# Kernel optimization log

Hardware: AMD Instinct MI355X
Metric: run time of the kernel (lower is better)

The kernel has to match this reference:

```python
import jax, jax.numpy as jnp
import numpy as np

MARGIN = 0.5   # arcface additive angular margin m
SCALE = 64.0   # arcface logit scale s
EPS = 1e-12    # torch F.normalize eps


def setup_inputs() -> dict:
    key = jax.random.key(0)
    k1, k2, k3 = jax.random.split(key, 3)
    B, D, C = 512, 512, 200000
    embeddings = jax.random.normal(k1, (B, D), dtype=jnp.float32)
    labels = jax.random.randint(k2, (B,), 0, C, dtype=jnp.int64)
    weight = 0.01 * jax.random.normal(k3, (C, D), dtype=jnp.float32)
    return {"embeddings": embeddings, "labels": labels, "weight": weight}


def _l2norm(x):
    # torch.nn.functional.normalize(x, dim=1): x / max(||x||, eps)
    n = jnp.sqrt(jnp.sum(x * x, axis=1, keepdims=True))
    return x / jnp.maximum(n, EPS)


def reference(embeddings, labels, weight):
    B = embeddings.shape[0]
    labels = labels.astype(jnp.int32)
    valid = labels >= 0                      # ignore_index=-1 semantics
    safe = jnp.where(valid, labels, 0)
    rows = jnp.arange(B)

    # normalize -> GEMM -> clamp
    logits = _l2norm(embeddings) @ _l2norm(weight).T   # [B, C] cosines
    logits = jnp.clip(logits, -1.0, 1.0)

    # arcface margin: target logit cos(theta) -> cos(theta + m)
    tgt = logits[rows, safe]
    theta = jnp.arccos(jnp.clip(tgt, -1.0 + 1e-7, 1.0 - 1e-7))
    new_tgt = jnp.cos(theta + MARGIN)
    logits = logits.at[rows, safe].set(jnp.where(valid, new_tgt, tgt))
    logits = logits * SCALE

    # cross entropy with ignore_index=-1, mean over valid
    logp = jax.nn.log_softmax(logits, axis=1)
    nll = -logp[rows, safe]
    n_valid = jnp.maximum(jnp.sum(valid.astype(jnp.float32)), 1.0)
    loss = jnp.sum(jnp.where(valid, nll, 0.0)) / n_valid
    return loss
```

## Files before the change

### kernel.cpp

```cpp
#include <hip/hip_runtime.h>
#include <hip/hip_bf16.h>


#define D_SZ 512
#define B_SZ 512
#define C_SZ 200000
#define BM   64
#define SCL  64.0f
#define MRG  0.5f

typedef __attribute__((ext_vector_type(8))) short  bf16x8;
typedef __attribute__((ext_vector_type(8))) __bf16 bf16x8f;
typedef __attribute__((ext_vector_type(4))) float  f32x4;

__device__ __forceinline__ ushort f2bf_bits(float x) {
  __bf16 h = (__bf16)x;
  return __builtin_bit_cast(ushort, h);
}

__device__ __forceinline__ bf16x8 cvt8(float4 a, float4 b) {
  bf16x8f t;
  t[0] = (__bf16)a.x; t[1] = (__bf16)a.y; t[2] = (__bf16)a.z; t[3] = (__bf16)a.w;
  t[4] = (__bf16)b.x; t[5] = (__bf16)b.y; t[6] = (__bf16)b.z; t[7] = (__bf16)b.w;
  return __builtin_bit_cast(bf16x8, t);
}

__global__ void k_norm_emb(const float* __restrict__ emb,
                           float* __restrict__ nf32,
                           ushort* __restrict__ nbf) {
  const int row  = blockIdx.x * 4 + (threadIdx.x >> 6);
  const int lane = threadIdx.x & 63;
  const float4* r4 = (const float4*)(emb + (size_t)row * D_SZ);
  float4 a = r4[lane];
  float4 b = r4[lane + 64];
  float ss = a.x*a.x + a.y*a.y + a.z*a.z + a.w*a.w
           + b.x*b.x + b.y*b.y + b.z*b.z + b.w*b.w;
#pragma unroll
  for (int off = 32; off; off >>= 1) ss += __shfl_xor(ss, off, 64);
  const float s = 1.0f / fmaxf(sqrtf(ss), 1e-12f);
  a.x *= s; a.y *= s; a.z *= s; a.w *= s;
  b.x *= s; b.y *= s; b.z *= s; b.w *= s;
  float4* o4 = (float4*)(nf32 + (size_t)row * D_SZ);
  o4[lane] = a; o4[lane + 64] = b;
  ushort4 ua, ub;
  ua.x = f2bf_bits(a.x); ua.y = f2bf_bits(a.y); ua.z = f2bf_bits(a.z); ua.w = f2bf_bits(a.w);
  ub.x = f2bf_bits(b.x); ub.y = f2bf_bits(b.y); ub.z = f2bf_bits(b.z); ub.w = f2bf_bits(b.w);
  ushort4* ob = (ushort4*)(nbf + (size_t)row * D_SZ);
  ob[lane] = ua; ob[lane + 64] = ub;
}

__global__ __launch_bounds__(512, 4)
void k_gemm_lse(const float* __restrict__ W,
                const ushort* __restrict__ E,
                float* __restrict__ gsum) {
  __shared__ ushort wtile[BM * D_SZ];
  __shared__ float  wlds[BM];
  const int tid  = threadIdx.x;
  const int wave = tid >> 6;
  const int lane = tid & 63;
  const size_t c0 = (size_t)blockIdx.x * BM;

  {
    const int r = tid >> 3, j = tid & 7;
    const float* wr = W + (c0 + r) * (size_t)D_SZ;
    char* wrow = (char*)wtile + r * (D_SZ * 2);
    const int sw = (r & 7) << 4;
    float wn = 0.f;
#pragma unroll
    for (int i = 0; i < 8; ++i) {
      const int cc = i * 8 + j;
      float4 x0 = *(const float4*)(wr + cc * 8);
      float4 x1 = *(const float4*)(wr + cc * 8 + 4);
      wn += x0.x*x0.x + x0.y*x0.y + x0.z*x0.z + x0.w*x0.w
          + x1.x*x1.x + x1.y*x1.y + x1.z*x1.z + x1.w*x1.w;
      *(bf16x8*)(wrow + ((cc * 16) ^ sw)) = cvt8(x0, x1);
    }
    wn += __shfl_xor(wn, 1, 64);
    wn += __shfl_xor(wn, 2, 64);
    wn += __shfl_xor(wn, 4, 64);
    if (j == 0) wlds[r] = wn;
  }
  __syncthreads();

  const int l15 = lane & 15;
  const int lk  = lane >> 4;
  const ushort* ebase = E + (size_t)(wave * 64 + l15) * D_SZ + lk * 8;
  const char*   abase = (const char*)wtile + l15 * (D_SZ * 2);
  const int     asw   = (l15 & 7) << 4;

  f32x4 acc[4][4];
  const f32x4 z = {0.f, 0.f, 0.f, 0.f};
#pragma unroll
  for (int ci = 0; ci < 4; ++ci)
#pragma unroll
    for (int bi = 0; bi < 4; ++bi) acc[ci][bi] = z;

#pragma unroll
  for (int ks = 0; ks < 16; ++ks) {
    bf16x8 wf[4], ef[4];
    const int ko = (ks * 64 + lk * 16) ^ asw;
#pragma unroll
    for (int ci = 0; ci < 4; ++ci)
      wf[ci] = *(const bf16x8*)(abase + ci * 16 * (D_SZ * 2) + ko);
#pragma unroll
    for (int bi = 0; bi < 4; ++bi)
      ef[bi] = *(const bf16x8*)(ebase + (size_t)(bi * 16) * D_SZ + ks * 32);
#pragma unroll
    for (int ci = 0; ci < 4; ++ci)
#pragma unroll
      for (int bi = 0; bi < 4; ++bi)
        acc[ci][bi] = __builtin_amdgcn_mfma_f32_16x16x32_bf16(
            wf[ci], ef[bi], acc[ci][bi], 0, 0, 0);
  }

  float psum[4] = {0.f, 0.f, 0.f, 0.f};
#pragma unroll
  for (int ci = 0; ci < 4; ++ci) {
#pragma unroll
    for (int r = 0; r < 4; ++r) {
      const float n2  = wlds[ci * 16 + lk * 4 + r];
      const float inv = 1.0f / fmaxf(sqrtf(n2), 1e-12f);
#pragma unroll
      for (int bi = 0; bi < 4; ++bi) {
        float c = acc[ci][bi][r] * inv;
        c = fminf(fmaxf(c, -1.0f), 1.0f);
        psum[bi] += __expf(fmaf(SCL, c, -SCL));
      }
    }
  }
#pragma unroll
  for (int bi = 0; bi < 4; ++bi) {
    psum[bi] += __shfl_xor(psum[bi], 16, 64);
    psum[bi] += __shfl_xor(psum[bi], 32, 64);
  }
  if (lk == 0) {
#pragma unroll
    for (int bi = 0; bi < 4; ++bi)
      atomicAdd(&gsum[wave * 64 + bi * 16 + l15], psum[bi]);
  }
}

__global__ void k_target(const float* __restrict__ W,
                         const float* __restrict__ nf32,
                         const int* __restrict__ labels,
                         const float* __restrict__ gsum,
                         float* __restrict__ nll) {
  const int wave = threadIdx.x >> 6;
  const int lane = threadIdx.x & 63;
  const int b = blockIdx.x * 8 + wave;
  const int lab = labels[b];
  const bool valid = (lab >= 0);
  const int slab = valid ? lab : 0;
  const float* wr = W    + (size_t)slab * D_SZ;
  const float* er = nf32 + (size_t)b    * D_SZ;
  float dot = 0.f, wn2 = 0.f;
#pragma unroll
  for (int i = 0; i < 2; ++i) {
    const int d = i * 256 + lane * 4;
    float4 w4 = *(const float4*)(wr + d);
    float4 e4 = *(const float4*)(er + d);
    dot += w4.x*e4.x + w4.y*e4.y + w4.z*e4.z + w4.w*e4.w;
    wn2 += w4.x*w4.x + w4.y*w4.y + w4.z*w4.z + w4.w*w4.w;
  }
#pragma unroll
  for (int off = 32; off; off >>= 1) {
    dot += __shfl_xor(dot, off, 64);
    wn2 += __shfl_xor(wn2, off, 64);
  }
  if (lane == 0 && valid) {
    const float inv  = 1.0f / fmaxf(sqrtf(wn2), 1e-12f);
    float cost = fminf(fmaxf(dot * inv, -1.0f), 1.0f);
    const float th   = acosf(fminf(fmaxf(cost, -1.0f + 1e-7f), 1.0f - 1e-7f));
    const float newt = cosf(th + MRG);
    const float sum  = gsum[b] - expf(fmaf(SCL, cost, -SCL))
                               + expf(fmaf(SCL, newt, -SCL));
    const float lse  = logf(sum) + SCL;
    atomicAdd(&nll[0], lse - SCL * newt);
    atomicAdd(&nll[1], 1.0f);
  }
}

__global__ void k_final(const float* __restrict__ nll, float* __restrict__ out) {
  out[0] = nll[0] / fmaxf(nll[1], 1.0f);
}

extern "C" void kernel_launch(void* const* d_in, const int* in_sizes, int n_in,
                              void* d_out, int out_size, void* d_ws, size_t ws_size,
                              hipStream_t stream) {
  const float* emb    = (const float*)d_in[0];
  const int*   labels = (const int*)  d_in[1];
  const float* W      = (const float*)d_in[2];
  float* out = (float*)d_out;

  char* ws = (char*)d_ws;
  float*  nf32 = (float*)ws;
  ushort* nbf  = (ushort*)(ws + (1u << 20));
  float*  gsum = (float*)(ws + (1u << 20) + (1u << 19));
  float*  nll  = gsum + B_SZ;

  hipMemsetAsync(gsum, 0, (B_SZ + 2) * sizeof(float), stream);
  k_norm_emb<<<B_SZ / 4, 256, 0, stream>>>(emb, nf32, nbf);
  k_gemm_lse<<<C_SZ / BM, 512, 0, stream>>>(W, nbf, gsum);
  k_target<<<B_SZ / 8, 512, 0, stream>>>(W, nf32, labels, gsum, nll);
  k_final<<<1, 1, 0, stream>>>(nll, out);
}
```

Before: 700.1 us.

## Double-buffer W chunks into LDS via async global_load_lds and overlap with MFMA

The GEMM kernel no longer loads the whole 64x512 W tile, converts it to bf16 and then syncs. It now streams four 128-column fp32 chunks into two LDS buffers with direct global-to-LDS loads, prefetching the next chunk while the current one feeds the MFMAs. The bf16 conversion and the row-norm accumulation now read from the fp32 LDS chunk. This is meant to hide global load latency behind compute. In exchange it doubles the LDS bytes read per element, adds conversion work inside the inner loop, and adds a barrier per chunk. The swizzle for global_load_lds depends on per-lane source addresses, which is a correctness risk.

```diff
diff --git a/kernel.cpp b/kernel.cpp
--- a/kernel.cpp
+++ b/kernel.cpp
@@ -6,6 +6,9 @@
 #define B_SZ 512
 #define C_SZ 200000
 #define BM   64
+#define CHK  128
+#define CHB  (CHK * 4)
+#define NCHK (D_SZ / CHK)
 #define SCL  64.0f
 #define MRG  0.5f
 
@@ -49,44 +52,37 @@
   ob[lane] = ua; ob[lane + 64] = ub;
 }
 
+__device__ __forceinline__ void stage_chunk(const float* __restrict__ W,
+                                            size_t c0, int ch, float* buf,
+                                            int wave, int lane) {
+  const int rl = lane >> 5;
+  const int cp = lane & 31;
+#pragma unroll
+  for (int i = 0; i < 4; ++i) {
+    const int r  = wave * 8 + 2 * i + rl;
+    const int cc = cp ^ (r & 7);
+    const float* src = W + (c0 + r) * (size_t)D_SZ + ch * CHK + cc * 4;
+    float* dst = buf + (wave * 8 + 2 * i) * CHK;
+    __builtin_amdgcn_global_load_lds(
+        (const __attribute__((address_space(1))) void*)src,
+        (__attribute__((address_space(3))) void*)dst, 16, 0, 0);
+  }
+}
+
 __global__ __launch_bounds__(512, 4)
 void k_gemm_lse(const float* __restrict__ W,
                 const ushort* __restrict__ E,
                 float* __restrict__ gsum) {
-  __shared__ ushort wtile[BM * D_SZ];
-  __shared__ float  wlds[BM];
+  __shared__ float bufs[2][BM * CHK];
+  __shared__ float wlds[BM];
   const int tid  = threadIdx.x;
   const int wave = tid >> 6;
   const int lane = tid & 63;
+  const int l15  = lane & 15;
+  const int lk   = lane >> 4;
   const size_t c0 = (size_t)blockIdx.x * BM;
-
-  {
-    const int r = tid >> 3, j = tid & 7;
-    const float* wr = W + (c0 + r) * (size_t)D_SZ;
-    char* wrow = (char*)wtile + r * (D_SZ * 2);
-    const int sw = (r & 7) << 4;
-    float wn = 0.f;
-#pragma unroll
-    for (int i = 0; i < 8; ++i) {
-      const int cc = i * 8 + j;
-      float4 x0 = *(const float4*)(wr + cc * 8);
-      float4 x1 = *(const float4*)(wr + cc * 8 + 4);
-      wn += x0.x*x0.x + x0.y*x0.y + x0.z*x0.z + x0.w*x0.w
-          + x1.x*x1.x + x1.y*x1.y + x1.z*x1.z + x1.w*x1.w;
-      *(bf16x8*)(wrow + ((cc * 16) ^ sw)) = cvt8(x0, x1);
-    }
-    wn += __shfl_xor(wn, 1, 64);
-    wn += __shfl_xor(wn, 2, 64);
-    wn += __shfl_xor(wn, 4, 64);
-    if (j == 0) wlds[r] = wn;
-  }
-  __syncthreads();
-
-  const int l15 = lane & 15;
-  const int lk  = lane >> 4;
   const ushort* ebase = E + (size_t)(wave * 64 + l15) * D_SZ + lk * 8;
-  const char*   abase = (const char*)wtile + l15 * (D_SZ * 2);
-  const int     asw   = (l15 & 7) << 4;
+  const int nr = tid >> 3, nj = tid & 7;
 
   f32x4 acc[4][4];
   const f32x4 z = {0.f, 0.f, 0.f, 0.f};
@@ -94,24 +90,58 @@
   for (int ci = 0; ci < 4; ++ci)
 #pragma unroll
     for (int bi = 0; bi < 4; ++bi) acc[ci][bi] = z;
-
-#pragma unroll
-  for (int ks = 0; ks < 16; ++ks) {
-    bf16x8 wf[4], ef[4];
-    const int ko = (ks * 64 + lk * 16) ^ asw;
-#pragma unroll
-    for (int ci = 0; ci < 4; ++ci)
-      wf[ci] = *(const bf16x8*)(abase + ci * 16 * (D_SZ * 2) + ko);
-#pragma unroll
-    for (int bi = 0; bi < 4; ++bi)
-      ef[bi] = *(const bf16x8*)(ebase + (size_t)(bi * 16) * D_SZ + ks * 32);
-#pragma unroll
-    for (int ci = 0; ci < 4; ++ci)
+  float wn = 0.f;
+
+  stage_chunk(W, c0, 0, bufs[0], wave, lane);
+  __syncthreads();
+
+#pragma unroll
+  for (int ch = 0; ch < NCHK; ++ch) {
+    float* cur = bufs[ch & 1];
+    if (ch + 1 < NCHK)
+      stage_chunk(W, c0, ch + 1, bufs[(ch + 1) & 1], wave, lane);
+
+    {
+      const char* rowp = (const char*)cur + nr * CHB;
+      const int sw2 = (nr & 7) << 4;
+#pragma unroll
+      for (int i = 0; i < 4; ++i) {
+        float4 x = *(const float4*)(rowp + (((i * 8 + nj) * 16) ^ sw2));
+        wn += x.x*x.x + x.y*x.y + x.z*x.z + x.w*x.w;
+      }
+    }
+
+    const int sw = (l15 & 7) << 4;
+#pragma unroll
+    for (int ks = 0; ks < 4; ++ks) {
+      bf16x8 wf[4], ef[4];
+      const int kb = ks * 128 + lk * 32;
+#pragma unroll
+      for (int ci = 0; ci < 4; ++ci) {
+        const char* rowp = (const char*)cur + (ci * 16 + l15) * CHB;
+        float4 x0 = *(const float4*)(rowp + (kb ^ sw));
+        float4 x1 = *(const float4*)(rowp + ((kb + 16) ^ sw));
+        wf[ci] = cvt8(x0, x1);
+      }
 #pragma unroll
       for (int bi = 0; bi < 4; ++bi)
-        acc[ci][bi] = __builtin_amdgcn_mfma_f32_16x16x32_bf16(
-            wf[ci], ef[bi], acc[ci][bi], 0, 0, 0);
-  }
+        ef[bi] = *(const bf16x8*)(ebase + (size_t)(bi * 16) * D_SZ
+                                  + ch * CHK + ks * 32);
+#pragma unroll
+      for (int ci = 0; ci < 4; ++ci)
+#pragma unroll
+        for (int bi = 0; bi < 4; ++bi)
+          acc[ci][bi] = __builtin_amdgcn_mfma_f32_16x16x32_bf16(
+              wf[ci], ef[bi], acc[ci][bi], 0, 0, 0);
+    }
+    __syncthreads();
+  }
+
+  wn += __shfl_xor(wn, 1, 64);
+  wn += __shfl_xor(wn, 2, 64);
+  wn += __shfl_xor(wn, 4, 64);
+  if (nj == 0) wlds[nr] = wn;
+  __syncthreads();
 
   float psum[4] = {0.f, 0.f, 0.f, 0.f};
 #pragma unroll
```

After: 867.9 us. +24.0%, slower.
